# Kernel optimization log

Hardware: AMD Instinct MI355X
Metric: run time of the kernel (lower is better)

## Reference

```python
import jax, jax.numpy as jnp
import numpy as np

N_NODES = 100000
N_FEAT = 256
N_HIDDEN = 64
N_EDGES = 3200000
LEAKY_SLOPE = 0.05


def setup_inputs() -> dict:
    key = jax.random.key(0)
    k1, k2, k3, k4, k5 = jax.random.split(key, 5)
    x = jax.random.normal(k1, (N_NODES, N_FEAT), dtype=jnp.float32)
    edge_index = jax.random.randint(k2, (2, N_EDGES), 0, N_NODES, dtype=jnp.int64)
    # params (torch Linear default-like scale)
    W_fc = jax.random.normal(k3, (N_FEAT, N_HIDDEN), dtype=jnp.float32) / np.sqrt(N_FEAT)
    a_w = jax.random.normal(k4, (2 * N_HIDDEN, 1), dtype=jnp.float32) / np.sqrt(2 * N_HIDDEN)
    a_b = jax.random.normal(k5, (1,), dtype=jnp.float32) * 0.01
    return {"x": x, "edge_index": edge_index, "W_fc": W_fc, "a_w": a_w, "a_b": a_b}


def reference(x, edge_index, W_fc, a_w, a_b):
    n = x.shape[0]
    h = x @ W_fc                                  # [N, H]
    src = edge_index[0]
    dst = edge_index[1]
    # a([h_src, h_dst]) == h_src @ a_w[:H] + h_dst @ a_w[H:] + a_b (same math, avoids concat)
    s = h @ a_w[:N_HIDDEN, 0]                     # [N]
    t = h @ a_w[N_HIDDEN:, 0]                     # [N]
    e = s[src] + t[dst] + a_b[0]                  # [E]
    e = jnp.where(e >= 0, e, LEAKY_SLOPE * e)     # LeakyReLU(0.05)
    attention = jnp.exp(e)                        # [E]
    row_sum = jax.ops.segment_sum(attention, src, num_segments=n)  # [N]
    alpha = attention / row_sum[src]              # [E]
    # sparse mm: out[i] = sum_{e: src_e=i} alpha_e * h[dst_e]
    out = jax.ops.segment_sum(alpha[:, None] * h[dst], src, num_segments=n)  # [N, H]
    return out, alpha
```

## Files before the change

kernel.cpp:

```cpp
#include <hip/hip_runtime.h>
#include <hip/hip_fp16.h>
#include <cstdint>
#include <cstddef>

#define NFEAT 256
#define NHID 64
#define SLOPE 0.05f
#define NBKT_MAX 392
#define P1 512
#define DSTBITS 17
#define WTPAD 264
#define SORTBUF 6272

typedef _Float16 half8 __attribute__((ext_vector_type(8)));
typedef float f32x4 __attribute__((ext_vector_type(4)));

__global__ __launch_bounds__(256) void fc_kernel(
    const float* __restrict__ x, const float* __restrict__ W,
    const float* __restrict__ aw,
    __half* __restrict__ h, float* __restrict__ srinv, float* __restrict__ t,
    int nNodes)
{
    __shared__ _Float16 Wt[NHID][WTPAD];

    const int tid = threadIdx.x;

    #pragma unroll 4
    for (int it = 0; it < 16; ++it) {
        const int idx = it * 256 + tid;
        const int n  = idx & 63;
        const int k0 = (idx >> 6) << 2;
        union { _Float16 v[4]; uint2 u; } pk;
        pk.v[0] = (_Float16)W[(k0 + 0) * NHID + n];
        pk.v[1] = (_Float16)W[(k0 + 1) * NHID + n];
        pk.v[2] = (_Float16)W[(k0 + 2) * NHID + n];
        pk.v[3] = (_Float16)W[(k0 + 3) * NHID + n];
        *(uint2*)&Wt[n][k0] = pk.u;
    }
    __syncthreads();

    const int l   = tid & 63;
    const int wv  = tid >> 6;
    const int l16 = l & 15;
    const int q   = l >> 4;
    const int kb8 = q * 8;

    const int blockRow = blockIdx.x * 128;
    const int nClamp = nNodes - 1;
    const int r0c = min(blockRow + wv * 32 + l16,      nClamp);
    const int r1c = min(blockRow + wv * 32 + l16 + 16, nClamp);
    const float* xr0 = x + (size_t)r0c * NFEAT;
    const float* xr1 = x + (size_t)r1c * NFEAT;

    f32x4 acc[2][4];
    #pragma unroll
    for (int m = 0; m < 2; ++m)
        #pragma unroll
        for (int nb = 0; nb < 4; ++nb)
            acc[m][nb] = (f32x4){0.f, 0.f, 0.f, 0.f};

    #pragma unroll
    for (int ks = 0; ks < 8; ++ks) {
        const int k0 = ks * 32 + kb8;
        const float4 fa0 = *(const float4*)(xr0 + k0);
        const float4 fa1 = *(const float4*)(xr0 + k0 + 4);
        const float4 fb0 = *(const float4*)(xr1 + k0);
        const float4 fb1 = *(const float4*)(xr1 + k0 + 4);
        half8 a0, a1;
        a0[0] = (_Float16)fa0.x; a0[1] = (_Float16)fa0.y;
        a0[2] = (_Float16)fa0.z; a0[3] = (_Float16)fa0.w;
        a0[4] = (_Float16)fa1.x; a0[5] = (_Float16)fa1.y;
        a0[6] = (_Float16)fa1.z; a0[7] = (_Float16)fa1.w;
        a1[0] = (_Float16)fb0.x; a1[1] = (_Float16)fb0.y;
        a1[2] = (_Float16)fb0.z; a1[3] = (_Float16)fb0.w;
        a1[4] = (_Float16)fb1.x; a1[5] = (_Float16)fb1.y;
        a1[6] = (_Float16)fb1.z; a1[7] = (_Float16)fb1.w;
        const half8 b0 = *(const half8*)&Wt[ 0 + l16][k0];
        const half8 b1 = *(const half8*)&Wt[16 + l16][k0];
        const half8 b2 = *(const half8*)&Wt[32 + l16][k0];
        const half8 b3 = *(const half8*)&Wt[48 + l16][k0];
        acc[0][0] = __builtin_amdgcn_mfma_f32_16x16x32_f16(a0, b0, acc[0][0], 0, 0, 0);
        acc[0][1] = __builtin_amdgcn_mfma_f32_16x16x32_f16(a0, b1, acc[0][1], 0, 0, 0);
        acc[0][2] = __builtin_amdgcn_mfma_f32_16x16x32_f16(a0, b2, acc[0][2], 0, 0, 0);
        acc[0][3] = __builtin_amdgcn_mfma_f32_16x16x32_f16(a0, b3, acc[0][3], 0, 0, 0);
        acc[1][0] = __builtin_amdgcn_mfma_f32_16x16x32_f16(a1, b0, acc[1][0], 0, 0, 0);
        acc[1][1] = __builtin_amdgcn_mfma_f32_16x16x32_f16(a1, b1, acc[1][1], 0, 0, 0);
        acc[1][2] = __builtin_amdgcn_mfma_f32_16x16x32_f16(a1, b2, acc[1][2], 0, 0, 0);
        acc[1][3] = __builtin_amdgcn_mfma_f32_16x16x32_f16(a1, b3, acc[1][3], 0, 0, 0);
    }

    const float aws0 = aw[l16],      aws1 = aw[16 + l16];
    const float aws2 = aw[32 + l16], aws3 = aw[48 + l16];
    const float awt0 = aw[64 + l16], awt1 = aw[80 + l16];
    const float awt2 = aw[96 + l16], awt3 = aw[112 + l16];

    #pragma unroll
    for (int m = 0; m < 2; ++m) {
        const int rb = blockRow + wv * 32 + m * 16 + q * 4;
        #pragma unroll
        for (int r = 0; r < 4; ++r) {
            const int row = rb + r;
            const bool ok = row < nNodes;
            const float c0 = acc[m][0][r];
            const float c1 = acc[m][1][r];
            const float c2 = acc[m][2][r];
            const float c3 = acc[m][3][r];
            if (ok) {
                __half* hp = &h[(size_t)row * NHID + l16];
                hp[0]  = __float2half(c0);
                hp[16] = __float2half(c1);
                hp[32] = __float2half(c2);
                hp[48] = __float2half(c3);
            }
            float ps = c0 * aws0 + c1 * aws1 + c2 * aws2 + c3 * aws3;
            float pt = c0 * awt0 + c1 * awt1 + c2 * awt2 + c3 * awt3;
            ps += __shfl_xor(ps, 1, 16); pt += __shfl_xor(pt, 1, 16);
            ps += __shfl_xor(ps, 2, 16); pt += __shfl_xor(pt, 2, 16);
            ps += __shfl_xor(ps, 4, 16); pt += __shfl_xor(pt, 4, 16);
            ps += __shfl_xor(ps, 8, 16); pt += __shfl_xor(pt, 8, 16);
            if (ok && l16 == 0) { srinv[2 * row] = ps; t[row] = pt; }
        }
    }
}

__global__ __launch_bounds__(256) void cnt_kernel(
    const int* __restrict__ ei, int E, int CPB, int nbkt, int* __restrict__ cntT)
{
    __shared__ int hist[NBKT_MAX];
    const int g = blockIdx.x;
    const int tid = threadIdx.x;
    for (int i = tid; i < nbkt; i += 256) hist[i] = 0;
    __syncthreads();
    const int beg = g * CPB;
    const int end = min(E, beg + CPB);
    const int c4 = (end - beg) >> 2;
    for (int i = tid; i < c4; i += 256) {
        const int4 v = *(const int4*)&ei[beg + i * 4];
        atomicAdd(&hist[v.x >> 8], 1);
        atomicAdd(&hist[v.y >> 8], 1);
        atomicAdd(&hist[v.z >> 8], 1);
        atomicAdd(&hist[v.w >> 8], 1);
    }
    for (int e = beg + c4 * 4 + tid; e < end; e += 256)
        atomicAdd(&hist[ei[e] >> 8], 1);
    __syncthreads();
    for (int b = tid; b < nbkt; b += 256)
        cntT[b * P1 + g] = hist[b];
}

__global__ __launch_bounds__(256) void scanA_kernel(
    const int* __restrict__ v, int* __restrict__ bsum, int n)
{
    __shared__ int sh[256];
    const int i = blockIdx.x * 256 + threadIdx.x;
    sh[threadIdx.x] = (i < n) ? v[i] : 0;
    __syncthreads();
    #pragma unroll
    for (int off = 128; off > 0; off >>= 1) {
        if (threadIdx.x < off) sh[threadIdx.x] += sh[threadIdx.x + off];
        __syncthreads();
    }
    if (threadIdx.x == 0) bsum[blockIdx.x] = sh[0];
}

__global__ __launch_bounds__(256) void scanC_kernel(
    const int* __restrict__ v, const int* __restrict__ bsum,
    int* __restrict__ outp, int n, int NB)
{
    __shared__ int red[256];
    __shared__ int sh[256];
    __shared__ int base0s;
    const int tid = threadIdx.x;

    int partial = 0;
    for (int j = tid; j < (int)blockIdx.x; j += 256) partial += bsum[j];
    red[tid] = partial;
    __syncthreads();
    #pragma unroll
    for (int off = 128; off > 0; off >>= 1) {
        if (tid < off) red[tid] += red[tid + off];
        __syncthreads();
    }
    if (tid == 0) base0s = red[0];
    __syncthreads();
    const int base0 = base0s;

    const int i = blockIdx.x * 256 + tid;
    const int val = (i < n) ? v[i] : 0;
    sh[tid] = val;
    __syncthreads();
    #pragma unroll
    for (int off = 1; off < 256; off <<= 1) {
        int add = (tid >= off) ? sh[tid - off] : 0;
        __syncthreads();
        sh[tid] += add;
        __syncthreads();
    }
    const int incl = sh[tid];
    if (i < n) outp[i] = base0 + incl - val;
    if (i == n - 1) outp[n] = base0 + incl;
}

__global__ __launch_bounds__(256) void place_kernel(
    const int* __restrict__ ei, int E, int CPB, int nbkt,
    const int* __restrict__ cntT, const int* __restrict__ base,
    int* __restrict__ pairs)
{
    __shared__ int loff[NBKT_MAX + 1];
    __shared__ int cur[NBKT_MAX];
    __shared__ int gb[NBKT_MAX];
    __shared__ int sorted[SORTBUF];

    const int g = blockIdx.x;
    const int tid = threadIdx.x;
    const int beg = g * CPB;
    const int end = min(E, beg + CPB);
    const int total = end - beg;

    for (int b = tid; b < nbkt; b += 256) {
        loff[b] = cntT[b * P1 + g];
        gb[b]   = base[b * P1 + g];
    }
    __syncthreads();
    if (tid == 0) {
        int run = 0;
        for (int b = 0; b < nbkt; ++b) { const int c = loff[b]; loff[b] = run; run += c; }
        loff[nbkt] = run;
    }
    __syncthreads();
    for (int b = tid; b < nbkt; b += 256) cur[b] = loff[b];
    __syncthreads();

    const int c4 = total >> 2;
    for (int i = tid; i < c4; i += 256) {
        const int e = beg + i * 4;
        const int4 s4 = *(const int4*)&ei[e];
        const int4 d4 = *(const int4*)&ei[E + e];
        int p;
        p = atomicAdd(&cur[s4.x >> 8], 1); sorted[p] = ((s4.x & 255) << DSTBITS) | d4.x;
        p = atomicAdd(&cur[s4.y >> 8], 1); sorted[p] = ((s4.y & 255) << DSTBITS) | d4.y;
        p = atomicAdd(&cur[s4.z >> 8], 1); sorted[p] = ((s4.z & 255) << DSTBITS) | d4.z;
        p = atomicAdd(&cur[s4.w >> 8], 1); sorted[p] = ((s4.w & 255) << DSTBITS) | d4.w;
    }
    for (int e = beg + c4 * 4 + tid; e < end; e += 256) {
        const int sn = ei[e];
        const int d  = ei[E + e];
        const int p  = atomicAdd(&cur[sn >> 8], 1);
        sorted[p] = ((sn & 255) << DSTBITS) | d;
    }
    __syncthreads();

    for (int i = tid; i < total; i += 256) {
        int lo = 0, hi = nbkt;
        #pragma unroll
        for (int it = 0; it < 9; ++it) {
            const int mid = (lo + hi) >> 1;
            if (loff[mid] <= i) lo = mid; else hi = mid;
        }
        pairs[gb[lo] + (i - loff[lo])] = sorted[i];
    }
}

__global__ __launch_bounds__(512) void bsort_kernel(
    const int* __restrict__ pairs, const int* __restrict__ base,
    int* __restrict__ offsets, int* __restrict__ sdst,
    int nNodes, int nbkt, int E)
{
    __shared__ int cnt[256];
    __shared__ int off[256];
    __shared__ int cur[256];

    const int bkt = blockIdx.x;
    const int tid = threadIdx.x;
    const int beg = base[bkt * P1];
    const int end = (bkt + 1 < nbkt) ? base[(bkt + 1) * P1] : E;

    if (tid < 256) cnt[tid] = 0;
    __syncthreads();

    for (int e = beg + tid; e < end; e += 512)
        atomicAdd(&cnt[pairs[e] >> DSTBITS], 1);
    __syncthreads();

    if (tid < 256) off[tid] = cnt[tid];
    __syncthreads();
    #pragma unroll
    for (int o = 1; o < 256; o <<= 1) {
        int v = 0;
        if (tid < 256 && tid >= o) v = off[tid - o];
        __syncthreads();
        if (tid < 256) off[tid] += v;
        __syncthreads();
    }
    if (tid < 256) {
        const int ex = off[tid] - cnt[tid];
        cur[tid] = ex;
        const int n = (bkt << 8) + tid;
        if (n < nNodes) offsets[n] = beg + ex;
    }
    if (tid == 0 && bkt == nbkt - 1) offsets[nNodes] = E;
    __syncthreads();

    for (int e = beg + tid; e < end; e += 512) {
        const int p = pairs[e];
        const int pos = beg + atomicAdd(&cur[p >> DSTBITS], 1);
        sdst[pos] = p & ((1 << DSTBITS) - 1);
    }
}

__global__ __launch_bounds__(256) void agg_kernel(
    const int* __restrict__ offsets, const int* __restrict__ sdst,
    float* __restrict__ srinv, const float* __restrict__ t,
    const __half* __restrict__ h, const float* __restrict__ ab_p,
    float* __restrict__ out, int nNodes)
{
    const int lane = threadIdx.x & 63;
    const int wv = threadIdx.x >> 6;
    const int quarter = lane >> 4;
    const int col = lane & 15;
    const float ab = ab_p[0];
    const int stride = gridDim.x * 4;
    const uint2* hh4 = (const uint2*)h;

    for (int n = blockIdx.x * 4 + wv; n < nNodes; n += stride) {
        const int beg = offsets[n];
        const int end = offsets[n + 1];
        const float sn = srinv[2 * n];
        float part = 0.f;
        float4 acc = {0.f, 0.f, 0.f, 0.f};
        for (int i0 = beg; i0 < end; i0 += 64) {
            const int my = min(end - i0, 64);
            int dl = 0; float el = 0.f;
            if (lane < my) {
                dl = sdst[i0 + lane];
                float ev = sn + t[dl] + ab;
                ev = (ev >= 0.f) ? ev : SLOPE * ev;
                el = __expf(ev);
            }
            part += el;
            const int my4 = (my + 3) & ~3;
            int j = 0;
            for (; j + 8 <= my4; j += 8) {
                const int   d0 = __shfl(dl, j + quarter);
                const float e0 = __shfl(el, j + quarter);
                const int   d1 = __shfl(dl, j + 4 + quarter);
                const float e1 = __shfl(el, j + 4 + quarter);
                const uint2 r0 = hh4[(size_t)d0 * 16 + col];
                const uint2 r1 = hh4[(size_t)d1 * 16 + col];
                const float2 lo0 = __half22float2(*(const __half2*)&r0.x);
                const float2 hi0 = __half22float2(*(const __half2*)&r0.y);
                const float2 lo1 = __half22float2(*(const __half2*)&r1.x);
                const float2 hi1 = __half22float2(*(const __half2*)&r1.y);
                acc.x += e0 * lo0.x; acc.y += e0 * lo0.y;
                acc.z += e0 * hi0.x; acc.w += e0 * hi0.y;
                acc.x += e1 * lo1.x; acc.y += e1 * lo1.y;
                acc.z += e1 * hi1.x; acc.w += e1 * hi1.y;
            }
            for (; j < my4; j += 4) {
                const int   d0 = __shfl(dl, j + quarter);
                const float e0 = __shfl(el, j + quarter);
                const uint2 r0 = hh4[(size_t)d0 * 16 + col];
                const float2 lo0 = __half22float2(*(const __half2*)&r0.x);
                const float2 hi0 = __half22float2(*(const __half2*)&r0.y);
                acc.x += e0 * lo0.x; acc.y += e0 * lo0.y;
                acc.z += e0 * hi0.x; acc.w += e0 * hi0.y;
            }
        }
        #pragma unroll
        for (int off = 32; off > 0; off >>= 1) part += __shfl_xor(part, off, 64);
        const float inv = (end > beg) ? 1.0f / part : 0.f;
        if (lane == 0) srinv[2 * n + 1] = inv;
        acc.x += __shfl_xor(acc.x, 16, 64); acc.x += __shfl_xor(acc.x, 32, 64);
        acc.y += __shfl_xor(acc.y, 16, 64); acc.y += __shfl_xor(acc.y, 32, 64);
        acc.z += __shfl_xor(acc.z, 16, 64); acc.z += __shfl_xor(acc.z, 32, 64);
        acc.w += __shfl_xor(acc.w, 16, 64); acc.w += __shfl_xor(acc.w, 32, 64);
        if (quarter == 0) {
            float4 o;
            o.x = acc.x * inv; o.y = acc.y * inv;
            o.z = acc.z * inv; o.w = acc.w * inv;
            *(float4*)&out[(size_t)n * NHID + col * 4] = o;
        }
    }
}

__global__ __launch_bounds__(256) void alpha_kernel(
    const int* __restrict__ ei, const float* __restrict__ srinv,
    const float* __restrict__ t,
    const float* __restrict__ ab_p, float* __restrict__ alpha, int E)
{
    const float ab = ab_p[0];
    const int gid = blockIdx.x * blockDim.x + threadIdx.x;
    const int step = gridDim.x * blockDim.x;
    const int E4 = E >> 2;

    #define AEDGE(sn, d) ({                                                 \
        const float2 sr = *(const float2*)&srinv[2 * (sn)];                 \
        float ev = sr.x + t[d] + ab;                                        \
        ev = (ev >= 0.f) ? ev : SLOPE * ev;                                 \
        __expf(ev) * sr.y; })

    for (int i = gid; i < E4; i += step) {
        const int e = i * 4;
        const int4 s4 = *(const int4*)&ei[e];
        const int4 d4 = *(const int4*)&ei[E + e];
        float4 a;
        a.x = AEDGE(s4.x, d4.x);
        a.y = AEDGE(s4.y, d4.y);
        a.z = AEDGE(s4.z, d4.z);
        a.w = AEDGE(s4.w, d4.w);
        *(float4*)&alpha[e] = a;
    }
    for (int e = E4 * 4 + gid; e < E; e += step) {
        const int sn = ei[e];
        const int d = ei[E + e];
        alpha[e] = AEDGE(sn, d);
    }
}

extern "C" void kernel_launch(void* const* d_in, const int* in_sizes, int n_in,
                              void* d_out, int out_size, void* d_ws, size_t ws_size,
                              hipStream_t stream)
{
    const float* x  = (const float*)d_in[0];
    const int*   ei = (const int*)d_in[1];
    const float* W  = (const float*)d_in[2];
    const float* aw = (const float*)d_in[3];
    const float* ab = (const float*)d_in[4];

    const int nNodes = in_sizes[0] / NFEAT;
    const int E      = in_sizes[1] / 2;
    const int NBfc   = (nNodes + 127) / 128;
    const int nbkt   = (nNodes + 255) >> 8;
    const int CPB    = ((E + P1 - 1) / P1 + 3) & ~3;
    const int nScan  = nbkt * P1;
    const int NBs    = (nScan + 255) / 256;

    float* out   = (float*)d_out;
    float* alpha = out + (size_t)nNodes * NHID;

    __half* h      = (__half*)d_ws;
    float* srinv   = (float*)(h + (size_t)nNodes * NHID);
    float* t       = srinv + 2 * nNodes;
    int*   cntT    = (int*)(t + nNodes);
    int*   base    = cntT + nScan;
    int*   bsum    = base + nScan + 4;
    int*   offsets = bsum + NBs;
    int*   sdst    = offsets + nNodes + 4;
    int*   pairs   = sdst + E;

    fc_kernel<<<NBfc, 256, 0, stream>>>(x, W, aw, h, srinv, t, nNodes);
    cnt_kernel<<<P1, 256, 0, stream>>>(ei, E, CPB, nbkt, cntT);
    scanA_kernel<<<NBs, 256, 0, stream>>>(cntT, bsum, nScan);
    scanC_kernel<<<NBs, 256, 0, stream>>>(cntT, bsum, base, nScan, NBs);
    place_kernel<<<P1, 256, 0, stream>>>(ei, E, CPB, nbkt, cntT, base, pairs);
    bsort_kernel<<<nbkt, 512, 0, stream>>>(pairs, base, offsets, sdst,
                                           nNodes, nbkt, E);
    agg_kernel<<<2048, 256, 0, stream>>>(offsets, sdst, srinv, t, h, ab,
                                         out, nNodes);
    alpha_kernel<<<2048, 256, 0, stream>>>(ei, srinv, t, ab, alpha, E);
}
```

Before: 175.3 us.

## Fuse bucket sort into aggregation using LDS-resident 128-node buckets

Buckets shrink from 256 to 128 source nodes so one bucket's edges fit in shared memory. The bucket sort and the aggregation become one kernel: each block counts, scans and scatters its edges into LDS, then aggregates straight from there. This drops the global offsets and sdst arrays and one launch. Each thread now holds at most ten edges in registers and the LDS buffer has a fixed capacity of 5120, so a bucket larger than that will produce wrong results. Aggregation runs on only about 782 blocks of 512 threads instead of a 2048-block grid-stride launch.

Result: no change. 172.7 us (-1.5%).

```diff
diff --git a/kernel.cpp b/kernel.cpp
--- a/kernel.cpp
+++ b/kernel.cpp
@@ -6,11 +6,13 @@
 #define NFEAT 256
 #define NHID 64
 #define SLOPE 0.05f
-#define NBKT_MAX 392
+#define BKTSZ 128
+#define NBKT_MAX 784
 #define P1 512
 #define DSTBITS 17
 #define WTPAD 264
 #define SORTBUF 6272
+#define BKTCAP 5120
 
 typedef _Float16 half8 __attribute__((ext_vector_type(8)));
 typedef float f32x4 __attribute__((ext_vector_type(4)));
@@ -136,13 +138,13 @@
     const int c4 = (end - beg) >> 2;
     for (int i = tid; i < c4; i += 256) {
         const int4 v = *(const int4*)&ei[beg + i * 4];
-        atomicAdd(&hist[v.x >> 8], 1);
-        atomicAdd(&hist[v.y >> 8], 1);
-        atomicAdd(&hist[v.z >> 8], 1);
-        atomicAdd(&hist[v.w >> 8], 1);
+        atomicAdd(&hist[v.x >> 7], 1);
+        atomicAdd(&hist[v.y >> 7], 1);
+        atomicAdd(&hist[v.z >> 7], 1);
+        atomicAdd(&hist[v.w >> 7], 1);
     }
     for (int e = beg + c4 * 4 + tid; e < end; e += 256)
-        atomicAdd(&hist[ei[e] >> 8], 1);
+        atomicAdd(&hist[ei[e] >> 7], 1);
     __syncthreads();
     for (int b = tid; b < nbkt; b += 256)
         cntT[b * P1 + g] = hist[b];
@@ -237,23 +239,23 @@
         const int4 s4 = *(const int4*)&ei[e];
         const int4 d4 = *(const int4*)&ei[E + e];
         int p;
-        p = atomicAdd(&cur[s4.x >> 8], 1); sorted[p] = ((s4.x & 255) << DSTBITS) | d4.x;
-        p = atomicAdd(&cur[s4.y >> 8], 1); sorted[p] = ((s4.y & 255) << DSTBITS) | d4.y;
-        p = atomicAdd(&cur[s4.z >> 8], 1); sorted[p] = ((s4.z & 255) << DSTBITS) | d4.z;
-        p = atomicAdd(&cur[s4.w >> 8], 1); sorted[p] = ((s4.w & 255) << DSTBITS) | d4.w;
+        p = atomicAdd(&cur[s4.x >> 7], 1); sorted[p] = ((s4.x & (BKTSZ-1)) << DSTBITS) | d4.x;
+        p = atomicAdd(&cur[s4.y >> 7], 1); sorted[p] = ((s4.y & (BKTSZ-1)) << DSTBITS) | d4.y;
+        p = atomicAdd(&cur[s4.z >> 7], 1); sorted[p] = ((s4.z & (BKTSZ-1)) << DSTBITS) | d4.z;
+        p = atomicAdd(&cur[s4.w >> 7], 1); sorted[p] = ((s4.w & (BKTSZ-1)) << DSTBITS) | d4.w;
     }
     for (int e = beg + c4 * 4 + tid; e < end; e += 256) {
         const int sn = ei[e];
         const int d  = ei[E + e];
-        const int p  = atomicAdd(&cur[sn >> 8], 1);
-        sorted[p] = ((sn & 255) << DSTBITS) | d;
+        const int p  = atomicAdd(&cur[sn >> 7], 1);
+        sorted[p] = ((sn & (BKTSZ-1)) << DSTBITS) | d;
     }
     __syncthreads();
 
     for (int i = tid; i < total; i += 256) {
         int lo = 0, hi = nbkt;
         #pragma unroll
-        for (int it = 0; it < 9; ++it) {
+        for (int it = 0; it < 10; ++it) {
             const int mid = (lo + hi) >> 1;
             if (loff[mid] <= i) lo = mid; else hi = mid;
         }
@@ -261,78 +263,82 @@
     }
 }
 
-__global__ __launch_bounds__(512) void bsort_kernel(
+__global__ __launch_bounds__(512) void bagg_kernel(
     const int* __restrict__ pairs, const int* __restrict__ base,
-    int* __restrict__ offsets, int* __restrict__ sdst,
-    int nNodes, int nbkt, int E)
-{
-    __shared__ int cnt[256];
-    __shared__ int off[256];
-    __shared__ int cur[256];
+    float* __restrict__ srinv, const float* __restrict__ t,
+    const __half* __restrict__ h, const float* __restrict__ ab_p,
+    float* __restrict__ out, int nNodes, int nbkt, int E)
+{
+    __shared__ int cnt[BKTSZ];
+    __shared__ int off[BKTSZ];
+    __shared__ int cur[BKTSZ];
+    __shared__ int sorted[BKTCAP];
 
     const int bkt = blockIdx.x;
     const int tid = threadIdx.x;
     const int beg = base[bkt * P1];
     const int end = (bkt + 1 < nbkt) ? base[(bkt + 1) * P1] : E;
 
-    if (tid < 256) cnt[tid] = 0;
-    __syncthreads();
-
-    for (int e = beg + tid; e < end; e += 512)
-        atomicAdd(&cnt[pairs[e] >> DSTBITS], 1);
-    __syncthreads();
-
-    if (tid < 256) off[tid] = cnt[tid];
-    __syncthreads();
-    #pragma unroll
-    for (int o = 1; o < 256; o <<= 1) {
+    if (tid < BKTSZ) cnt[tid] = 0;
+    __syncthreads();
+
+    int pr[10];
+    int myc = 0;
+    #pragma unroll
+    for (int k = 0; k < 10; ++k) {
+        const int e = beg + k * 512 + tid;
+        if (e < end) {
+            const int p = pairs[e];
+            pr[k] = p;
+            atomicAdd(&cnt[p >> DSTBITS], 1);
+            myc = k + 1;
+        }
+    }
+    __syncthreads();
+
+    if (tid < BKTSZ) off[tid] = cnt[tid];
+    __syncthreads();
+    #pragma unroll
+    for (int o = 1; o < BKTSZ; o <<= 1) {
         int v = 0;
-        if (tid < 256 && tid >= o) v = off[tid - o];
-        __syncthreads();
-        if (tid < 256) off[tid] += v;
-        __syncthreads();
-    }
-    if (tid < 256) {
-        const int ex = off[tid] - cnt[tid];
-        cur[tid] = ex;
-        const int n = (bkt << 8) + tid;
-        if (n < nNodes) offsets[n] = beg + ex;
-    }
-    if (tid == 0 && bkt == nbkt - 1) offsets[nNodes] = E;
-    __syncthreads();
-
-    for (int e = beg + tid; e < end; e += 512) {
-        const int p = pairs[e];
-        const int pos = beg + atomicAdd(&cur[p >> DSTBITS], 1);
-        sdst[pos] = p & ((1 << DSTBITS) - 1);
-    }
-}
-
-__global__ __launch_bounds__(256) void agg_kernel(
-    const int* __restrict__ offsets, const int* __restrict__ sdst,
-    float* __restrict__ srinv, const float* __restrict__ t,
-    const __half* __restrict__ h, const float* __restrict__ ab_p,
-    float* __restrict__ out, int nNodes)
-{
-    const int lane = threadIdx.x & 63;
-    const int wv = threadIdx.x >> 6;
+        if (tid < BKTSZ && tid >= o) v = off[tid - o];
+        __syncthreads();
+        if (tid < BKTSZ) off[tid] += v;
+        __syncthreads();
+    }
+    if (tid < BKTSZ) cur[tid] = off[tid] - cnt[tid];
+    __syncthreads();
+
+    #pragma unroll
+    for (int k = 0; k < 10; ++k) {
+        if (k < myc) {
+            const int p = pr[k];
+            const int pos = atomicAdd(&cur[p >> DSTBITS], 1);
+            sorted[pos] = p & ((1 << DSTBITS) - 1);
+        }
+    }
+    __syncthreads();
+
+    const int lane = tid & 63;
+    const int wv = tid >> 6;
     const int quarter = lane >> 4;
     const int col = lane & 15;
     const float ab = ab_p[0];
-    const int stride = gridDim.x * 4;
     const uint2* hh4 = (const uint2*)h;
 
-    for (int n = blockIdx.x * 4 + wv; n < nNodes; n += stride) {
-        const int beg = offsets[n];
-        const int end = offsets[n + 1];
+    for (int li = wv; li < BKTSZ; li += 8) {
+        const int n = (bkt << 7) + li;
+        if (n >= nNodes) continue;
+        const int endL = off[li];
+        const int begL = endL - cnt[li];
         const float sn = srinv[2 * n];
         float part = 0.f;
         float4 acc = {0.f, 0.f, 0.f, 0.f};
-        for (int i0 = beg; i0 < end; i0 += 64) {
-            const int my = min(end - i0, 64);
+        for (int i0 = begL; i0 < endL; i0 += 64) {
+            const int my = min(endL - i0, 64);
             int dl = 0; float el = 0.f;
             if (lane < my) {
-                dl = sdst[i0 + lane];
+                dl = sorted[i0 + lane];
                 float ev = sn + t[dl] + ab;
                 ev = (ev >= 0.f) ? ev : SLOPE * ev;
                 el = __expf(ev);
@@ -367,18 +373,18 @@
             }
         }
         #pragma unroll
-        for (int off = 32; off > 0; off >>= 1) part += __shfl_xor(part, off, 64);
-        const float inv = (end > beg) ? 1.0f / part : 0.f;
+        for (int o = 32; o > 0; o >>= 1) part += __shfl_xor(part, o, 64);
+        const float inv = (endL > begL) ? 1.0f / part : 0.f;
         if (lane == 0) srinv[2 * n + 1] = inv;
         acc.x += __shfl_xor(acc.x, 16, 64); acc.x += __shfl_xor(acc.x, 32, 64);
         acc.y += __shfl_xor(acc.y, 16, 64); acc.y += __shfl_xor(acc.y, 32, 64);
         acc.z += __shfl_xor(acc.z, 16, 64); acc.z += __shfl_xor(acc.z, 32, 64);
         acc.w += __shfl_xor(acc.w, 16, 64); acc.w += __shfl_xor(acc.w, 32, 64);
         if (quarter == 0) {
-            float4 o;
-            o.x = acc.x * inv; o.y = acc.y * inv;
-            o.z = acc.z * inv; o.w = acc.w * inv;
-            *(float4*)&out[(size_t)n * NHID + col * 4] = o;
+            float4 o4;
+            o4.x = acc.x * inv; o4.y = acc.y * inv;
+            o4.z = acc.z * inv; o4.w = acc.w * inv;
+            *(float4*)&out[(size_t)n * NHID + col * 4] = o4;
         }
     }
 }
@@ -430,7 +436,7 @@
     const int nNodes = in_sizes[0] / NFEAT;
     const int E      = in_sizes[1] / 2;
     const int NBfc   = (nNodes + 127) / 128;
-    const int nbkt   = (nNodes + 255) >> 8;
+    const int nbkt   = (nNodes + BKTSZ - 1) / BKTSZ;
     const int CPB    = ((E + P1 - 1) / P1 + 3) & ~3;
     const int nScan  = nbkt * P1;
     const int NBs    = (nScan + 255) / 256;
@@ -444,18 +450,14 @@
     int*   cntT    = (int*)(t + nNodes);
     int*   base    = cntT + nScan;
     int*   bsum    = base + nScan + 4;
-    int*   offsets = bsum + NBs;
-    int*   sdst    = offsets + nNodes + 4;
-    int*   pairs   = sdst + E;
+    int*   pairs   = bsum + NBs;
 
     fc_kernel<<<NBfc, 256, 0, stream>>>(x, W, aw, h, srinv, t, nNodes);
     cnt_kernel<<<P1, 256, 0, stream>>>(ei, E, CPB, nbkt, cntT);
     scanA_kernel<<<NBs, 256, 0, stream>>>(cntT, bsum, nScan);
     scanC_kernel<<<NBs, 256, 0, stream>>>(cntT, bsum, base, nScan, NBs);
     place_kernel<<<P1, 256, 0, stream>>>(ei, E, CPB, nbkt, cntT, base, pairs);
-    bsort_kernel<<<nbkt, 512, 0, stream>>>(pairs, base, offsets, sdst,
-                                           nNodes, nbkt, E);
-    agg_kernel<<<2048, 256, 0, stream>>>(offsets, sdst, srinv, t, h, ab,
-                                         out, nNodes);
+    bagg_kernel<<<nbkt, 512, 0, stream>>>(pairs, base, srinv, t, h, ab,
+                                          out, nNodes, nbkt, E);
     alpha_kernel<<<2048, 256, 0, stream>>>(ei, srinv, t, ab, alpha, E);
 }
```
